# Performance work log

Measured on AMD Instinct MI355X. Metric: run time of the kernel, lower is better.

## Reference

```python
import jax, jax.numpy as jnp
import numpy as np

N = 524288   # total graph nodes
V = 64       # number of virtual nodes (clusters)
C = N // V   # nodes per cluster (8192)
D = 256      # in_feats
H = 256      # hidden_feats
EPS = 1e-5


def setup_inputs() -> dict:
    key = jax.random.key(0)
    ks = jax.random.split(key, 8)
    sD = 1.0 / np.sqrt(D)
    sH = 1.0 / np.sqrt(2 * H)
    inp = {
        "x": jax.random.normal(ks[0], (N, D), dtype=jnp.float32),
        "vn_emb": jax.random.normal(ks[1], (V, D), dtype=jnp.float32) * 0.1,
        "wq": jax.random.normal(ks[2], (D, D), dtype=jnp.float32) * sD,
        "wk": jax.random.normal(ks[3], (D, D), dtype=jnp.float32) * sD,
        "v_attn": jax.random.normal(ks[4], (D,), dtype=jnp.float32) * sD,
        "w1": jax.random.normal(ks[5], (D, 2 * H), dtype=jnp.float32) * sD,
        "b1": jnp.zeros((2 * H,), dtype=jnp.float32),
        "g1": jnp.ones((2 * H,), dtype=jnp.float32),
        "beta1": jnp.zeros((2 * H,), dtype=jnp.float32),
        "w2": jax.random.normal(ks[6], (2 * H, H), dtype=jnp.float32) * sH,
        "b2": jnp.zeros((H,), dtype=jnp.float32),
        "g2": jnp.ones((H,), dtype=jnp.float32),
        "beta2": jnp.zeros((H,), dtype=jnp.float32),
        # cluster v owns contiguous node block [v*C, (v+1)*C)
        "vn_index": jnp.arange(N, dtype=jnp.int32).reshape(V, C),
        "vn_indices": jnp.stack(
            [jnp.arange(N, dtype=jnp.int32), (jnp.arange(N, dtype=jnp.int32) // C)],
            axis=1),
    }
    return inp


def _batchnorm(z, g, b):
    # training-mode BN over the virtual-node batch dim
    m = jnp.mean(z, axis=0)
    v = jnp.var(z, axis=0)
    return (z - m) * jax.lax.rsqrt(v + EPS) * g + b


def reference(x, vn_emb, wq, wk, v_attn, w1, b1, g1, beta1,
              w2, b2, g2, beta2, vn_index, vn_indices):
    vx = vn_emb                                   # [V, D]
    # --- update_node_emb (layer 0): broadcast-add VN emb to its nodes ---
    h = x + vx[vn_indices[:, 1]]                  # [N, D]
    # --- update_vn_emb: per-cluster additive attention pooling (vectorized over V) ---
    cluster_h = h[vn_index]                       # [V, C, D]
    q = vx @ wq                                   # [V, D]
    kproj = jnp.einsum('vcd,de->vce', cluster_h, wk)   # [V, C, D]
    scores = jnp.einsum('vce,e->vc', jnp.tanh(kproj + q[:, None, :]), v_attn)
    attn = jax.nn.softmax(scores, axis=-1)        # [V, C]
    pooled = jnp.einsum('vc,vcd->vd', attn, cluster_h) + vx  # [V, D]
    # --- mlp_vns[0]: Linear -> BN -> ReLU -> Linear -> BN -> ReLU ---
    z = jax.nn.relu(_batchnorm(pooled @ w1 + b1, g1, beta1))  # [V, 2H]
    vx_new = jax.nn.relu(_batchnorm(z @ w2 + b2, g2, beta2))  # [V, H]
    return h, vx_new
```

## Files before the change

### kernel.cpp

```cpp
#include <hip/hip_runtime.h>


typedef __bf16 bf16x8 __attribute__((ext_vector_type(8)));
typedef float f32x4 __attribute__((ext_vector_type(4)));
typedef unsigned short us8 __attribute__((ext_vector_type(8)));

__device__ __forceinline__ unsigned short f2bf(float f) {
  unsigned int u = __float_as_uint(f);
  return (unsigned short)((u + 0x7fffu + ((u >> 16) & 1u)) >> 16);
}
__device__ __forceinline__ float tanh_fast(float x) {
  float cx = fminf(fmaxf(x, -15.f), 15.f);
  float e = __expf(2.f * cx);
  return (e - 1.f) * __builtin_amdgcn_rcpf(e + 1.f);
}
__device__ __forceinline__ float wave_sum(float v) {
#pragma unroll
  for (int o = 1; o < 64; o <<= 1) v += __shfl_xor(v, o);
  return v;
}
__device__ __forceinline__ void lgkm_barrier() {
  asm volatile("s_waitcnt lgkmcnt(0)" ::: "memory");
  __builtin_amdgcn_sched_barrier(0);
  __builtin_amdgcn_s_barrier();
  __builtin_amdgcn_sched_barrier(0);
}
__device__ __forceinline__ void gll16(const float* gp, float* lp) {
  __builtin_amdgcn_global_load_lds(
      (const __attribute__((address_space(1))) void*)gp,
      (__attribute__((address_space(3))) void*)lp, 16, 0, 0);
}

__global__ __launch_bounds__(256) void k_prep(
    const float* __restrict__ vn_emb, const float* __restrict__ wq,
    const float* __restrict__ wk, float* __restrict__ qg,
    unsigned short* __restrict__ wkp) {
  int t = threadIdx.x;
  int b = blockIdx.x;
  if (b < 64) {
    float a = 0.f;
#pragma unroll 4
    for (int d = 0; d < 256; ++d) a += vn_emb[(b << 8) + d] * wq[(d << 8) + t];
    qg[(b << 8) + t] = a;
  } else {
    int tid = ((b - 64) << 8) + t;
    int l = tid & 63;
    int ks = (tid >> 6) & 7;
    int ct = tid >> 9;
    int col = (ct << 4) + (l & 15);
    int d0 = (ks << 5) + ((l >> 4) << 3);
    us8 o;
#pragma unroll
    for (int e = 0; e < 8; ++e) o[e] = f2bf(wk[(d0 + e) * 256 + col]);
    *reinterpret_cast<us8*>(wkp + (size_t)tid * 8) = o;
  }
}

__global__ __launch_bounds__(1024) void k_main16(
    const float* __restrict__ x, const float* __restrict__ vn_emb,
    const float* __restrict__ v_attn, const float* __restrict__ qg,
    const unsigned short* __restrict__ wkp, float* __restrict__ hout,
    float* __restrict__ vecs, float* __restrict__ Zb) {
  __shared__ float stage[2][32 * 256];
  __shared__ unsigned short hs[32 * 256];
  __shared__ float vxs[256], qv[256], va[256];
  __shared__ float spbuf[16][32];

  const int t = threadIdx.x;
  const int blk = blockIdx.x;
  const int cl = blk >> 2;

  if (t < 256) {
    vxs[t] = vn_emb[(cl << 8) + t];
    qv[t] = qg[(cl << 8) + t];
    va[t] = v_attn[t];
  }

  const int l = t & 63, wv = t >> 6;
  const int lr = l & 15, lg = l >> 4;
  const int ct = wv;
  const int srow0 = wv << 1;

  bf16x8 wkf[8];
#pragma unroll
  for (int ks = 0; ks < 8; ++ks)
    wkf[ks] = __builtin_bit_cast(
        bf16x8, *reinterpret_cast<const us8*>(
                    wkp + ((size_t)((((ct << 3) + ks) << 6) + l)) * 8));

  char* hsb = reinterpret_cast<char*>(hs);
  const size_t growbase = ((size_t)blk << 11) + srow0;

  f32x4 acc = {0.f, 0.f, 0.f, 0.f};
  float zacc = 0.f;

#pragma unroll
  for (int tt = 0; tt < 2; ++tt)
#pragma unroll
    for (int i = 0; i < 2; ++i)
      gll16(x + (((growbase + (tt << 5) + i) << 8) + (l << 2)),
            &stage[tt][(srow0 + i) << 8]);

  __syncthreads();

  const f32x4 vv = *reinterpret_cast<const f32x4*>(&vxs[l << 2]);
  const int eo0 = (ct << 4) + (lg << 2);
  const f32x4 qf = *reinterpret_cast<const f32x4*>(&qv[eo0]);
  const f32x4 vf = *reinterpret_cast<const f32x4*>(&va[eo0]);
  f32x4 hh0, hh1;

  for (int tile = 0; tile < 64; ++tile) {
    if (tile == 63) {
      asm volatile("s_waitcnt vmcnt(0)" ::: "memory");
    } else {
      asm volatile("s_waitcnt vmcnt(2)" ::: "memory");
    }
    __builtin_amdgcn_sched_barrier(0);

    const float* sb = &stage[tile & 1][0];
    const size_t hg0 = ((growbase + ((size_t)tile << 5)) << 8) + (l << 2);
#define S1(hhX, i)                                                          \
  {                                                                         \
    f32x4 sv = *reinterpret_cast<const f32x4*>(                             \
        &sb[((srow0 + i) << 8) + (l << 2)]);                                \
    hhX = sv + vv;                                                          \
    *reinterpret_cast<f32x4*>(hout + hg0 + ((size_t)i << 8)) = hhX;         \
    ushort4 o;                                                              \
    o.x = f2bf(hhX[0]);                                                     \
    o.y = f2bf(hhX[1]);                                                     \
    o.z = f2bf(hhX[2]);                                                     \
    o.w = f2bf(hhX[3]);                                                     \
    int row = srow0 + i;                                                    \
    *reinterpret_cast<ushort4*>(                                            \
        hsb + ((row << 9) + ((l << 3) ^ ((row & 7) << 4)))) = o;            \
  }
    S1(hh0, 0) S1(hh1, 1)
#undef S1

    __builtin_amdgcn_sched_barrier(0);
    if (tile < 62) {
      const int tt = tile + 2;
#pragma unroll
      for (int i = 0; i < 2; ++i)
        gll16(x + (((growbase + ((size_t)tt << 5) + i) << 8) + (l << 2)),
              &stage[tile & 1][(srow0 + i) << 8]);
    }
    lgkm_barrier();

#pragma unroll
    for (int rg = 0; rg < 2; ++rg) {
      bf16x8 bfr[8];
      {
        int row2 = (rg << 4) + lr;
        int sw = (row2 & 7) << 4;
#pragma unroll
        for (int ks = 0; ks < 8; ++ks)
          bfr[ks] = __builtin_bit_cast(
              bf16x8,
              *reinterpret_cast<const us8*>(
                  hsb + ((row2 << 9) + ((((ks << 6) + (lg << 4))) ^ sw))));
      }
      f32x4 ac0 = {0.f, 0.f, 0.f, 0.f};
#pragma unroll
      for (int ks = 0; ks < 8; ++ks)
        ac0 = __builtin_amdgcn_mfma_f32_16x16x32_bf16(wkf[ks], bfr[ks], ac0, 0,
                                                      0, 0);
      float sp = 0.f;
#pragma unroll
      for (int r = 0; r < 4; ++r) sp += tanh_fast(ac0[r] + qf[r]) * vf[r];
      sp += __shfl_xor(sp, 16);
      sp += __shfl_xor(sp, 32);
      if (lg == 0) spbuf[ct][(rg << 4) + lr] = sp;
    }
    lgkm_barrier();

    float srow = 0.f;
    if (l < 32) {
#pragma unroll
      for (int q = 0; q < 16; ++q) srow += spbuf[q][l];
    }
    float w_all = __expf(srow);
    if (wv == 0 && l < 32) zacc += w_all;
    {
      float wn0 = __shfl(w_all, srow0 + 0);
      float wn1 = __shfl(w_all, srow0 + 1);
      acc += wn0 * hh0 + wn1 * hh1;
    }
  }

  __syncthreads();
  float* sc = reinterpret_cast<float*>(hs);
  *reinterpret_cast<f32x4*>(&sc[(wv << 8) + (l << 2)]) = acc;
  __syncthreads();
  if (t < 256) {
    float s = 0.f;
#pragma unroll
    for (int w16 = 0; w16 < 16; ++w16) s += sc[(w16 << 8) + t];
    vecs[((size_t)blk << 8) + t] = s;
  }
  if (wv == 0) {
    float z = wave_sum(zacc);
    if (l == 0) Zb[blk] = z;
  }
}

__global__ __launch_bounds__(256) void k_combine(
    const float* __restrict__ vecs, const float* __restrict__ Zb,
    const float* __restrict__ vn_emb, float* __restrict__ pooledT) {
  int v = blockIdx.x, t = threadIdx.x;
  float s = 0.f, z = 0.f;
#pragma unroll
  for (int b = 0; b < 4; ++b) {
    s += vecs[(size_t)(((v << 2) + b) << 8) + t];
    z += Zb[(v << 2) + b];
  }
  pooledT[(t << 6) + v] = s / z + vn_emb[(v << 8) + t];
}

__global__ __launch_bounds__(64) void k_mlp1(
    const float* __restrict__ pooledT, const float* __restrict__ w1,
    const float* __restrict__ b1, const float* __restrict__ g1,
    const float* __restrict__ be1, float* __restrict__ z1T) {
  int j = blockIdx.x, v = threadIdx.x;
  float a = 0.f;
#pragma unroll 4
  for (int d = 0; d < 256; ++d) a += pooledT[(d << 6) + v] * w1[(d << 9) + j];
  a += b1[j];
  float mu = wave_sum(a) * (1.f / 64.f);
  float df = a - mu;
  float var = wave_sum(df * df) * (1.f / 64.f);
  float z = df * rsqrtf(var + 1e-5f) * g1[j] + be1[j];
  z1T[(j << 6) + v] = fmaxf(z, 0.f);
}

__global__ __launch_bounds__(64) void k_mlp2(
    const float* __restrict__ z1T, const float* __restrict__ w2,
    const float* __restrict__ b2, const float* __restrict__ g2,
    const float* __restrict__ be2, float* __restrict__ vout) {
  int j = blockIdx.x, v = threadIdx.x;
  float a = 0.f;
#pragma unroll 4
  for (int k = 0; k < 512; ++k) a += z1T[(k << 6) + v] * w2[(k << 8) + j];
  a += b2[j];
  float mu = wave_sum(a) * (1.f / 64.f);
  float df = a - mu;
  float var = wave_sum(df * df) * (1.f / 64.f);
  float z = df * rsqrtf(var + 1e-5f) * g2[j] + be2[j];
  vout[(v << 8) + j] = fmaxf(z, 0.f);
}

extern "C" void kernel_launch(void* const* d_in, const int* in_sizes, int n_in,
                              void* d_out, int out_size, void* d_ws,
                              size_t ws_size, hipStream_t stream) {
  const float* x = (const float*)d_in[0];
  const float* vn_emb = (const float*)d_in[1];
  const float* wq = (const float*)d_in[2];
  const float* wk = (const float*)d_in[3];
  const float* v_attn = (const float*)d_in[4];
  const float* w1 = (const float*)d_in[5];
  const float* b1 = (const float*)d_in[6];
  const float* g1 = (const float*)d_in[7];
  const float* beta1 = (const float*)d_in[8];
  const float* w2 = (const float*)d_in[9];
  const float* b2 = (const float*)d_in[10];
  const float* g2 = (const float*)d_in[11];
  const float* beta2 = (const float*)d_in[12];

  char* wsb = (char*)d_ws;
  float* qg = (float*)(wsb + 0);
  unsigned short* wkp = (unsigned short*)(wsb + 65536);
  float* vecs = (float*)(wsb + 196608);
  float* Zb = (float*)(wsb + 458752);
  float* pooledT = (float*)(wsb + 462848);
  float* z1T = (float*)(wsb + 528384);

  float* hout = (float*)d_out;
  float* vout = hout + (size_t)524288 * 256;

  k_prep<<<96, 256, 0, stream>>>(vn_emb, wq, wk, qg, wkp);
  k_main16<<<256, 1024, 0, stream>>>(x, vn_emb, v_attn, qg, wkp, hout, vecs,
                                     Zb);
  k_combine<<<64, 256, 0, stream>>>(vecs, Zb, vn_emb, pooledT);
  k_mlp1<<<512, 64, 0, stream>>>(pooledT, w1, b1, g1, beta1, z1T);
  k_mlp2<<<256, 64, 0, stream>>>(z1T, w2, b2, g2, beta2, vout);
}
```

Before: 324.4 us.

## Split main kernel into 512 half-size blocks with two column tiles per wave

Replaces the 256-block, 1024-thread main kernel with 512 blocks of 512 threads. Each block handles 16-row tiles instead of 32, and each wave now owns two column tiles of the key projection. The aim is to halve shared memory per block so more blocks fit on each CU, fill all CUs, and reduce barrier cost per block. The trade-offs are twice the per-wave register use for the held wk fragments and twice as many partial sums for the combine kernel to reduce.

```diff
diff --git a/kernel.cpp b/kernel.cpp
--- a/kernel.cpp
+++ b/kernel.cpp
@@ -56,19 +56,19 @@
   }
 }
 
-__global__ __launch_bounds__(1024) void k_main16(
+__global__ __launch_bounds__(512, 4) void k_main2b(
     const float* __restrict__ x, const float* __restrict__ vn_emb,
     const float* __restrict__ v_attn, const float* __restrict__ qg,
     const unsigned short* __restrict__ wkp, float* __restrict__ hout,
     float* __restrict__ vecs, float* __restrict__ Zb) {
-  __shared__ float stage[2][32 * 256];
-  __shared__ unsigned short hs[32 * 256];
+  __shared__ float stage[2][16 * 256];
+  __shared__ unsigned short hs[16 * 256];
   __shared__ float vxs[256], qv[256], va[256];
-  __shared__ float spbuf[16][32];
+  __shared__ float spbuf[8][16];
 
   const int t = threadIdx.x;
   const int blk = blockIdx.x;
-  const int cl = blk >> 2;
+  const int cl = blk >> 3;
 
   if (t < 256) {
     vxs[t] = vn_emb[(cl << 8) + t];
@@ -78,18 +78,21 @@
 
   const int l = t & 63, wv = t >> 6;
   const int lr = l & 15, lg = l >> 4;
-  const int ct = wv;
   const int srow0 = wv << 1;
 
-  bf16x8 wkf[8];
-#pragma unroll
-  for (int ks = 0; ks < 8; ++ks)
-    wkf[ks] = __builtin_bit_cast(
-        bf16x8, *reinterpret_cast<const us8*>(
-                    wkp + ((size_t)((((ct << 3) + ks) << 6) + l)) * 8));
+  bf16x8 wkf[2][8];
+#pragma unroll
+  for (int c = 0; c < 2; ++c)
+#pragma unroll
+    for (int ks = 0; ks < 8; ++ks) {
+      const int ct = (wv << 1) + c;
+      wkf[c][ks] = __builtin_bit_cast(
+          bf16x8, *reinterpret_cast<const us8*>(
+                      wkp + ((size_t)((((ct << 3) + ks) << 6) + l)) * 8));
+    }
 
   char* hsb = reinterpret_cast<char*>(hs);
-  const size_t growbase = ((size_t)blk << 11) + srow0;
+  const size_t growbase = ((size_t)blk << 10) + srow0;
 
   f32x4 acc = {0.f, 0.f, 0.f, 0.f};
   float zacc = 0.f;
@@ -98,15 +101,12 @@
   for (int tt = 0; tt < 2; ++tt)
 #pragma unroll
     for (int i = 0; i < 2; ++i)
-      gll16(x + (((growbase + (tt << 5) + i) << 8) + (l << 2)),
+      gll16(x + (((growbase + (tt << 4) + i) << 8) + (l << 2)),
             &stage[tt][(srow0 + i) << 8]);
 
   __syncthreads();
 
   const f32x4 vv = *reinterpret_cast<const f32x4*>(&vxs[l << 2]);
-  const int eo0 = (ct << 4) + (lg << 2);
-  const f32x4 qf = *reinterpret_cast<const f32x4*>(&qv[eo0]);
-  const f32x4 vf = *reinterpret_cast<const f32x4*>(&va[eo0]);
   f32x4 hh0, hh1;
 
   for (int tile = 0; tile < 64; ++tile) {
@@ -118,7 +118,7 @@
     __builtin_amdgcn_sched_barrier(0);
 
     const float* sb = &stage[tile & 1][0];
-    const size_t hg0 = ((growbase + ((size_t)tile << 5)) << 8) + (l << 2);
+    const size_t hg0 = ((growbase + ((size_t)tile << 4)) << 8) + (l << 2);
 #define S1(hhX, i)                                                          \
   {                                                                         \
     f32x4 sv = *reinterpret_cast<const f32x4*>(                             \
@@ -142,45 +142,49 @@
       const int tt = tile + 2;
 #pragma unroll
       for (int i = 0; i < 2; ++i)
-        gll16(x + (((growbase + ((size_t)tt << 5) + i) << 8) + (l << 2)),
+        gll16(x + (((growbase + ((size_t)tt << 4) + i) << 8) + (l << 2)),
               &stage[tile & 1][(srow0 + i) << 8]);
     }
     lgkm_barrier();
 
-#pragma unroll
-    for (int rg = 0; rg < 2; ++rg) {
-      bf16x8 bfr[8];
-      {
-        int row2 = (rg << 4) + lr;
-        int sw = (row2 & 7) << 4;
-#pragma unroll
-        for (int ks = 0; ks < 8; ++ks)
-          bfr[ks] = __builtin_bit_cast(
-              bf16x8,
-              *reinterpret_cast<const us8*>(
-                  hsb + ((row2 << 9) + ((((ks << 6) + (lg << 4))) ^ sw))));
-      }
+    bf16x8 bfr[8];
+    {
+      const int sw = (lr & 7) << 4;
+#pragma unroll
+      for (int ks = 0; ks < 8; ++ks)
+        bfr[ks] = __builtin_bit_cast(
+            bf16x8, *reinterpret_cast<const us8*>(
+                        hsb + ((lr << 9) + ((((ks << 6) + (lg << 4))) ^ sw))));
+    }
+    float spt = 0.f;
+#pragma unroll
+    for (int c = 0; c < 2; ++c) {
+      const int ct = (wv << 1) + c;
       f32x4 ac0 = {0.f, 0.f, 0.f, 0.f};
 #pragma unroll
       for (int ks = 0; ks < 8; ++ks)
-        ac0 = __builtin_amdgcn_mfma_f32_16x16x32_bf16(wkf[ks], bfr[ks], ac0, 0,
-                                                      0, 0);
+        ac0 = __builtin_amdgcn_mfma_f32_16x16x32_bf16(wkf[c][ks], bfr[ks], ac0,
+                                                      0, 0, 0);
+      const int eo0 = (ct << 4) + (lg << 2);
+      const f32x4 qf = *reinterpret_cast<const f32x4*>(&qv[eo0]);
+      const f32x4 vf = *reinterpret_cast<const f32x4*>(&va[eo0]);
       float sp = 0.f;
 #pragma unroll
       for (int r = 0; r < 4; ++r) sp += tanh_fast(ac0[r] + qf[r]) * vf[r];
-      sp += __shfl_xor(sp, 16);
-      sp += __shfl_xor(sp, 32);
-      if (lg == 0) spbuf[ct][(rg << 4) + lr] = sp;
-    }
+      spt += sp;
+    }
+    spt += __shfl_xor(spt, 16);
+    spt += __shfl_xor(spt, 32);
+    if (l < 16) spbuf[wv][l] = spt;
     lgkm_barrier();
 
     float srow = 0.f;
-    if (l < 32) {
-#pragma unroll
-      for (int q = 0; q < 16; ++q) srow += spbuf[q][l];
+    if (l < 16) {
+#pragma unroll
+      for (int q = 0; q < 8; ++q) srow += spbuf[q][l];
     }
     float w_all = __expf(srow);
-    if (wv == 0 && l < 32) zacc += w_all;
+    if (wv == 0 && l < 16) zacc += w_all;
     {
       float wn0 = __shfl(w_all, srow0 + 0);
       float wn1 = __shfl(w_all, srow0 + 1);
@@ -195,7 +199,7 @@
   if (t < 256) {
     float s = 0.f;
 #pragma unroll
-    for (int w16 = 0; w16 < 16; ++w16) s += sc[(w16 << 8) + t];
+    for (int w8 = 0; w8 < 8; ++w8) s += sc[(w8 << 8) + t];
     vecs[((size_t)blk << 8) + t] = s;
   }
   if (wv == 0) {
@@ -210,9 +214,9 @@
   int v = blockIdx.x, t = threadIdx.x;
   float s = 0.f, z = 0.f;
 #pragma unroll
-  for (int b = 0; b < 4; ++b) {
-    s += vecs[(size_t)(((v << 2) + b) << 8) + t];
-    z += Zb[(v << 2) + b];
+  for (int b = 0; b < 8; ++b) {
+    s += vecs[(size_t)(((v << 3) + b) << 8) + t];
+    z += Zb[(v << 3) + b];
   }
   pooledT[(t << 6) + v] = s / z + vn_emb[(v << 8) + t];
 }
@@ -270,16 +274,16 @@
   float* qg = (float*)(wsb + 0);
   unsigned short* wkp = (unsigned short*)(wsb + 65536);
   float* vecs = (float*)(wsb + 196608);
-  float* Zb = (float*)(wsb + 458752);
-  float* pooledT = (float*)(wsb + 462848);
-  float* z1T = (float*)(wsb + 528384);
+  float* Zb = (float*)(wsb + 720896);
+  float* pooledT = (float*)(wsb + 722944);
+  float* z1T = (float*)(wsb + 788480);
 
   float* hout = (float*)d_out;
   float* vout = hout + (size_t)524288 * 256;
 
   k_prep<<<96, 256, 0, stream>>>(vn_emb, wq, wk, qg, wkp);
-  k_main16<<<256, 1024, 0, stream>>>(x, vn_emb, v_attn, qg, wkp, hout, vecs,
-                                     Zb);
+  k_main2b<<<512, 512, 0, stream>>>(x, vn_emb, v_attn, qg, wkp, hout, vecs,
+                                    Zb);
   k_combine<<<64, 256, 0, stream>>>(vecs, Zb, vn_emb, pooledT);
   k_mlp1<<<512, 64, 0, stream>>>(pooledT, w1, b1, g1, beta1, z1T);
   k_mlp2<<<256, 64, 0, stream>>>(z1T, w2, b2, g2, beta2, vout);
```

Result: slower. 515.6 us (+58.9%).
